# Optimization experiments

Hardware: AMD Instinct MI355X
Metric: run time of the kernel (lower is better)

Reference implementation:

```python
import jax, jax.numpy as jnp
import numpy as np

LMAX = 6
IN_F = 128
OUT_F = 128
B = 16384
M = (LMAX + 1) ** 2  # 49


def _make_expand_index(lmax):
    idx = np.zeros((lmax + 1) ** 2, dtype=np.int64)
    for l in range(lmax + 1):
        idx[l * l : l * l + 2 * l + 1] = l
    return jnp.asarray(idx)


def setup_inputs() -> dict:
    key = jax.random.key(0)
    k1, k2 = jax.random.split(key)
    bound = 1.0 / np.sqrt(IN_F)
    inputs = jax.random.normal(k1, (B, M, IN_F), dtype=jnp.float32)
    weight = jax.random.uniform(k2, (LMAX + 1, OUT_F, IN_F), dtype=jnp.float32,
                                minval=-bound, maxval=bound)
    bias = jnp.zeros((1, 1, OUT_F), dtype=jnp.float32)
    expand_index = _make_expand_index(LMAX)
    return {"inputs": inputs, "weight": weight, "bias": bias,
            "expand_index": expand_index}


def reference(inputs, weight, bias, expand_index):
    # expand per-l weights to per-m weights: [M, out, in]
    w = jnp.take(weight, expand_index, axis=0)
    # batched per-m matmul: [B, M, in] x [M, out, in] -> [B, M, out]
    out = jnp.einsum('bmi,moi->bmo', inputs, w)
    # bias only on the l=0 (m=0) component
    out = out.at[:, 0:1, :].add(bias)
    return out
```

## Files before the change

kernel.cpp:

```cpp
#include <hip/hip_runtime.h>
#include <hip/hip_bf16.h>

#define MDIM 49
#define INF 128
#define OUTF 128
#define BDIM 16384
#define BT 64
#define TILES_PER_BLOCK 4
#define BLOCKS_PER_M (BDIM / (BT * TILES_PER_BLOCK))

typedef __attribute__((ext_vector_type(8))) short bf16x8;
typedef __attribute__((ext_vector_type(4))) float f32x4;

static __device__ __forceinline__ short f2bf(float f) {
  __hip_bfloat16 h = __float2bfloat16(f);
  union { __hip_bfloat16 h; unsigned short u; } c;
  c.h = h;
  return (short)c.u;
}

static __device__ __forceinline__ bf16x8 cvt8(f32x4 a, f32x4 b) {
  bf16x8 r;
  r[0] = f2bf(a[0]); r[1] = f2bf(a[1]); r[2] = f2bf(a[2]); r[3] = f2bf(a[3]);
  r[4] = f2bf(b[0]); r[5] = f2bf(b[1]); r[6] = f2bf(b[2]); r[7] = f2bf(b[3]);
  return r;
}

__global__ __launch_bounds__(256) void so3_linear_kernel(
    const float* __restrict__ in, const float* __restrict__ wt,
    const float* __restrict__ bias, float* __restrict__ out) {
  const int m    = blockIdx.x;
  const int blk  = blockIdx.y;
  const int tid  = threadIdx.x;
  const int lane = tid & 63;
  const int wv   = tid >> 6;

  int l = 0;
  while ((l + 1) * (l + 1) <= m) ++l;

  __shared__ short lds[BT][INF + 8];

  const int colbase = wv * 32;
  const int col0    = colbase + (lane & 15);
  const int krow    = (lane >> 4) * 8;
  const float* wl   = wt + (size_t)l * OUTF * INF;
  bf16x8 wfrag[2][4];
#pragma unroll
  for (int ot = 0; ot < 2; ++ot) {
    const float* wp = wl + (size_t)(col0 + ot * 16) * INF + krow;
#pragma unroll
    for (int ks = 0; ks < 4; ++ks) {
      f32x4 w0 = *(const f32x4*)(wp + ks * 32);
      f32x4 w1 = *(const f32x4*)(wp + ks * 32 + 4);
      wfrag[ot][ks] = cvt8(w0, w1);
    }
  }
  f32x4 biasadd[2];
#pragma unroll
  for (int ot = 0; ot < 2; ++ot) {
    biasadd[ot] = (m == 0) ? *(const f32x4*)(bias + colbase + ot * 16 + (lane >> 4) * 4)
                           : (f32x4){0.f, 0.f, 0.f, 0.f};
  }

  const int c8 = (tid & 15) * 8;
  const int r0 = tid >> 4;
  const int b0 = blk * (TILES_PER_BLOCK * BT);

  const size_t rowstride = (size_t)MDIM * INF;

  f32x4 pf[8];
  {
    const float* ip = in + ((size_t)(b0 + r0) * MDIM + m) * INF + c8;
#pragma unroll
    for (int p = 0; p < 4; ++p) {
      pf[2 * p]     = *(const f32x4*)(ip + p * 16 * rowstride);
      pf[2 * p + 1] = *(const f32x4*)(ip + p * 16 * rowstride + 4);
    }
  }

  for (int tt = 0; tt < TILES_PER_BLOCK; ++tt) {
#pragma unroll
    for (int p = 0; p < 4; ++p) {
      *(bf16x8*)&lds[r0 + 16 * p][c8] = cvt8(pf[2 * p], pf[2 * p + 1]);
    }
    __syncthreads();

    if (tt + 1 < TILES_PER_BLOCK) {
      const float* ip =
          in + ((size_t)(b0 + (tt + 1) * BT + r0) * MDIM + m) * INF + c8;
#pragma unroll
      for (int p = 0; p < 4; ++p) {
        pf[2 * p]     = *(const f32x4*)(ip + p * 16 * rowstride);
        pf[2 * p + 1] = *(const f32x4*)(ip + p * 16 * rowstride + 4);
      }
    }

    f32x4 acc[4][2];
#pragma unroll
    for (int bt = 0; bt < 4; ++bt)
#pragma unroll
      for (int ot = 0; ot < 2; ++ot)
        acc[bt][ot] = (f32x4){0.f, 0.f, 0.f, 0.f};

#pragma unroll
    for (int bt = 0; bt < 4; ++bt) {
      const int arow = bt * 16 + (lane & 15);
#pragma unroll
      for (int ks = 0; ks < 4; ++ks) {
        bf16x8 a = *(const bf16x8*)&lds[arow][ks * 32 + krow];
        acc[bt][0] = __builtin_amdgcn_mfma_f32_16x16x32_bf16(
            wfrag[0][ks], a, acc[bt][0], 0, 0, 0);
        acc[bt][1] = __builtin_amdgcn_mfma_f32_16x16x32_bf16(
            wfrag[1][ks], a, acc[bt][1], 0, 0, 0);
      }
    }

    const int btile = b0 + tt * BT;
#pragma unroll
    for (int bt = 0; bt < 4; ++bt) {
      const int b = btile + bt * 16 + (lane & 15);
      float* op = out + ((size_t)b * MDIM + m) * OUTF + colbase + (lane >> 4) * 4;
#pragma unroll
      for (int ot = 0; ot < 2; ++ot) {
        f32x4 v = acc[bt][ot];
        v[0] += biasadd[ot][0]; v[1] += biasadd[ot][1];
        v[2] += biasadd[ot][2]; v[3] += biasadd[ot][3];
        *(f32x4*)(op + ot * 16) = v;
      }
    }
    __syncthreads();
  }
}

extern "C" void kernel_launch(void* const* d_in, const int* in_sizes, int n_in,
                              void* d_out, int out_size, void* d_ws, size_t ws_size,
                              hipStream_t stream) {
  const float* in   = (const float*)d_in[0];
  const float* wt   = (const float*)d_in[1];
  const float* bias = (const float*)d_in[2];
  float* out        = (float*)d_out;
  dim3 grid(MDIM, BLOCKS_PER_M);
  so3_linear_kernel<<<grid, dim3(256), 0, stream>>>(in, wt, bias, out);
}
```

Before: 184.1 us.

## Load input fragments directly into registers, dropping LDS staging and barriers

Each wave now reads its 16-row input fragments straight from global memory into MFMA operand registers, with a register prefetch of the next step, instead of staging a 64-row tile through shared memory. This removes the LDS writes, LDS reads and both block barriers per tile. In exchange, all four waves in a block read the same input rows, so global/L2 load traffic for the input quadruples, and each step does less MFMA work per load.

```diff
diff --git a/kernel.cpp b/kernel.cpp
--- a/kernel.cpp
+++ b/kernel.cpp
@@ -5,9 +5,9 @@
 #define INF 128
 #define OUTF 128
 #define BDIM 16384
-#define BT 64
-#define TILES_PER_BLOCK 4
-#define BLOCKS_PER_M (BDIM / (BT * TILES_PER_BLOCK))
+#define ROWS 16
+#define T_PER_BLK 16
+#define BLOCKS_PER_M (BDIM / (ROWS * T_PER_BLK))
 
 typedef __attribute__((ext_vector_type(8))) short bf16x8;
 typedef __attribute__((ext_vector_type(4))) float f32x4;
@@ -38,97 +38,75 @@
   int l = 0;
   while ((l + 1) * (l + 1) <= m) ++l;
 
-  __shared__ short lds[BT][INF + 8];
+  const int colbase = wv * 32;
+  const int r16     = lane & 15;
+  const int koff    = (lane >> 4) * 8;
 
-  const int colbase = wv * 32;
-  const int col0    = colbase + (lane & 15);
-  const int krow    = (lane >> 4) * 8;
-  const float* wl   = wt + (size_t)l * OUTF * INF;
+  const float* wl = wt + (size_t)l * OUTF * INF;
   bf16x8 wfrag[2][4];
 #pragma unroll
-  for (int ot = 0; ot < 2; ++ot) {
-    const float* wp = wl + (size_t)(col0 + ot * 16) * INF + krow;
+  for (int ct = 0; ct < 2; ++ct) {
+    const float* wp = wl + (size_t)(colbase + ct * 16 + r16) * INF + koff;
 #pragma unroll
     for (int ks = 0; ks < 4; ++ks) {
       f32x4 w0 = *(const f32x4*)(wp + ks * 32);
       f32x4 w1 = *(const f32x4*)(wp + ks * 32 + 4);
-      wfrag[ot][ks] = cvt8(w0, w1);
-    }
-  }
-  f32x4 biasadd[2];
-#pragma unroll
-  for (int ot = 0; ot < 2; ++ot) {
-    biasadd[ot] = (m == 0) ? *(const f32x4*)(bias + colbase + ot * 16 + (lane >> 4) * 4)
-                           : (f32x4){0.f, 0.f, 0.f, 0.f};
-  }
-
-  const int c8 = (tid & 15) * 8;
-  const int r0 = tid >> 4;
-  const int b0 = blk * (TILES_PER_BLOCK * BT);
-
-  const size_t rowstride = (size_t)MDIM * INF;
-
-  f32x4 pf[8];
-  {
-    const float* ip = in + ((size_t)(b0 + r0) * MDIM + m) * INF + c8;
-#pragma unroll
-    for (int p = 0; p < 4; ++p) {
-      pf[2 * p]     = *(const f32x4*)(ip + p * 16 * rowstride);
-      pf[2 * p + 1] = *(const f32x4*)(ip + p * 16 * rowstride + 4);
+      wfrag[ct][ks] = cvt8(w0, w1);
     }
   }
 
-  for (int tt = 0; tt < TILES_PER_BLOCK; ++tt) {
+  f32x4 biasadd[2];
 #pragma unroll
-    for (int p = 0; p < 4; ++p) {
-      *(bf16x8*)&lds[r0 + 16 * p][c8] = cvt8(pf[2 * p], pf[2 * p + 1]);
-    }
-    __syncthreads();
+  for (int ct = 0; ct < 2; ++ct) {
+    biasadd[ct] = (m == 0)
+        ? *(const f32x4*)(bias + colbase + ct * 16 + (lane >> 4) * 4)
+        : (f32x4){0.f, 0.f, 0.f, 0.f};
+  }
 
-    if (tt + 1 < TILES_PER_BLOCK) {
-      const float* ip =
-          in + ((size_t)(b0 + (tt + 1) * BT + r0) * MDIM + m) * INF + c8;
+  const size_t rowstride = (size_t)MDIM * INF;
+  const int b0 = blk * (T_PER_BLK * ROWS);
+
+  const float* ip0 = in + ((size_t)(b0 + r16) * rowstride) + (size_t)m * INF + koff;
+
+  f32x4 pf[8];
 #pragma unroll
-      for (int p = 0; p < 4; ++p) {
-        pf[2 * p]     = *(const f32x4*)(ip + p * 16 * rowstride);
-        pf[2 * p + 1] = *(const f32x4*)(ip + p * 16 * rowstride + 4);
+  for (int ks = 0; ks < 4; ++ks) {
+    pf[2 * ks]     = *(const f32x4*)(ip0 + ks * 32);
+    pf[2 * ks + 1] = *(const f32x4*)(ip0 + ks * 32 + 4);
+  }
+
+  for (int t = 0; t < T_PER_BLK; ++t) {
+    bf16x8 xfrag[4];
+#pragma unroll
+    for (int ks = 0; ks < 4; ++ks) xfrag[ks] = cvt8(pf[2 * ks], pf[2 * ks + 1]);
+
+    if (t + 1 < T_PER_BLK) {
+      const float* ip = ip0 + (size_t)(t + 1) * ROWS * rowstride;
+#pragma unroll
+      for (int ks = 0; ks < 4; ++ks) {
+        pf[2 * ks]     = *(const f32x4*)(ip + ks * 32);
+        pf[2 * ks + 1] = *(const f32x4*)(ip + ks * 32 + 4);
       }
     }
 
-    f32x4 acc[4][2];
+    f32x4 acc[2];
+    acc[0] = (f32x4){0.f, 0.f, 0.f, 0.f};
+    acc[1] = (f32x4){0.f, 0.f, 0.f, 0.f};
 #pragma unroll
-    for (int bt = 0; bt < 4; ++bt)
-#pragma unroll
-      for (int ot = 0; ot < 2; ++ot)
-        acc[bt][ot] = (f32x4){0.f, 0.f, 0.f, 0.f};
-
-#pragma unroll
-    for (int bt = 0; bt < 4; ++bt) {
-      const int arow = bt * 16 + (lane & 15);
-#pragma unroll
-      for (int ks = 0; ks < 4; ++ks) {
-        bf16x8 a = *(const bf16x8*)&lds[arow][ks * 32 + krow];
-        acc[bt][0] = __builtin_amdgcn_mfma_f32_16x16x32_bf16(
-            wfrag[0][ks], a, acc[bt][0], 0, 0, 0);
-        acc[bt][1] = __builtin_amdgcn_mfma_f32_16x16x32_bf16(
-            wfrag[1][ks], a, acc[bt][1], 0, 0, 0);
-      }
+    for (int ks = 0; ks < 4; ++ks) {
+      acc[0] = __builtin_amdgcn_mfma_f32_16x16x32_bf16(wfrag[0][ks], xfrag[ks], acc[0], 0, 0, 0);
+      acc[1] = __builtin_amdgcn_mfma_f32_16x16x32_bf16(wfrag[1][ks], xfrag[ks], acc[1], 0, 0, 0);
     }
 
-    const int btile = b0 + tt * BT;
+    const int b = b0 + t * ROWS + r16;
+    float* op = out + (size_t)b * rowstride + (size_t)m * OUTF + colbase + (lane >> 4) * 4;
 #pragma unroll
-    for (int bt = 0; bt < 4; ++bt) {
-      const int b = btile + bt * 16 + (lane & 15);
-      float* op = out + ((size_t)b * MDIM + m) * OUTF + colbase + (lane >> 4) * 4;
-#pragma unroll
-      for (int ot = 0; ot < 2; ++ot) {
-        f32x4 v = acc[bt][ot];
-        v[0] += biasadd[ot][0]; v[1] += biasadd[ot][1];
-        v[2] += biasadd[ot][2]; v[3] += biasadd[ot][3];
-        *(f32x4*)(op + ot * 16) = v;
-      }
+    for (int ct = 0; ct < 2; ++ct) {
+      f32x4 v = acc[ct];
+      v[0] += biasadd[ct][0]; v[1] += biasadd[ct][1];
+      v[2] += biasadd[ct][2]; v[3] += biasadd[ct][3];
+      *(f32x4*)(op + ct * 16) = v;
     }
-    __syncthreads();
   }
 }
 
```

New measurement: 287.2 us. 1.56x slower.
